# Optimization experiments

Measured on AMD Instinct MI355X. Metric: run time of the kernel, lower is better.

Reference implementation:

```python
import jax, jax.numpy as jnp
import numpy as np

WS = (4, 4, 4)          # window size (s, h, w)
NUM_HEADS = 6
DIM = 192               # kv channels C
CS = 2                  # channel_scale; q/out channels = DIM // CS
B = 256                 # num_windows * batch


def _rel_pos_index(ws):
    """Reproduces the module's relative_position_index buffer (shape [8shw, 2shw])."""
    s, h, w = ws
    cs = np.repeat(np.arange(s), 2)
    ch = np.repeat(np.arange(h), 2)
    cw = np.repeat(np.arange(w), 2)
    coords = np.stack(np.meshgrid(cs, ch, cw, indexing='ij'))   # (3, 2s, 2h, 2w)
    cf = coords.reshape(3, -1)                                   # (3, T), T = 8shw
    rel = cf[:, :, None] - cf[:, None, :]                        # (3, T, T)
    rel = rel[:, :, ::4]                                         # (3, T, T//4)
    rel = np.ascontiguousarray(rel.transpose(1, 2, 0))           # (T, T//4, 3)
    rel[:, :, 0] += s - 1
    rel[:, :, 1] += h - 1
    rel[:, :, 2] += w - 1
    rel[:, :, 0] *= 3 * h - 1
    rel[:, :, 1] *= 2 * h - 1
    return rel.sum(-1).astype(np.int32)                          # (T, T//4)


def setup_inputs() -> dict:
    key = jax.random.key(0)
    ks = jax.random.split(key, 9)
    s, h, w = WS
    qN = 8 * s * h * w          # 512 query tokens per window
    N = qN // 4                 # 128 key/value tokens per window
    C = DIM
    qC = DIM // CS
    table_len = (4 * s - 1) * (4 * h - 1) * (4 * w - 1)
    return {
        'kv': jax.random.normal(ks[0], (B, N, C), jnp.float32),
        'q': jax.random.normal(ks[1], (B, qN, qC), jnp.float32),
        'w_kv': jax.random.normal(ks[2], (C, 2 * C), jnp.float32) * 0.02,
        'b_kv': jnp.zeros((2 * C,), jnp.float32),
        'w_q': jax.random.normal(ks[3], (qC, C), jnp.float32) * 0.02,
        'b_q': jnp.zeros((C,), jnp.float32),
        'w_proj': jax.random.normal(ks[4], (C, qC), jnp.float32) * 0.02,
        'b_proj': jnp.zeros((qC,), jnp.float32),
        'bias_table': jax.random.normal(ks[5], (table_len, NUM_HEADS), jnp.float32) * 0.02,
        'rel_index': jnp.asarray(_rel_pos_index(WS)),
    }


def reference(kv, q, w_kv, b_kv, w_q, b_q, w_proj, b_proj, bias_table, rel_index):
    B_, N, C = kv.shape
    d = C // NUM_HEADS
    scale = d ** -0.5
    # project kv -> k, v : (B_, nH, N, d)
    kvp = (kv @ w_kv + b_kv).reshape(B_, N, 2, NUM_HEADS, d)
    k = kvp[:, :, 0].transpose(0, 2, 1, 3)
    v = kvp[:, :, 1].transpose(0, 2, 1, 3)
    # project q : (B_, nH, qN, d), pre-scaled
    qp = (q @ w_q + b_q).reshape(B_, -1, NUM_HEADS, d).transpose(0, 2, 1, 3) * scale
    attn = jnp.einsum('bhqd,bhkd->bhqk', qp, k)          # (B_, nH, qN, N)
    bias = bias_table[rel_index]                          # (qN, N, nH) gather
    attn = attn + bias.transpose(2, 0, 1)[None]           # + (1, nH, qN, N)
    attn = jax.nn.softmax(attn, axis=-1)
    out = jnp.einsum('bhqk,bhkd->bhqd', attn, v)          # (B_, nH, qN, d)
    out = out.transpose(0, 2, 1, 3).reshape(B_, -1, C)    # (B_, qN, C)
    return out @ w_proj + b_proj                          # (B_, qN, C//CS)
```

## Files before the change

### kernel.cpp

```cpp
#include <hip/hip_runtime.h>
#include <hip/hip_bf16.h>

#define B_    256
#define NKV   128
#define NQ    512
#define CDIM  192
#define QCDIM 96
#define NH    6
#define DH    32
#define SCALE 0.17677669529663687f

typedef __hip_bfloat16 bf16;
typedef __attribute__((ext_vector_type(8))) short s16x8;
typedef __attribute__((ext_vector_type(4))) float f32x4;
#define MFMA16(a, b, c) __builtin_amdgcn_mfma_f32_16x16x32_bf16(a, b, c, 0, 0, 0)

#define OFF_BIASF 0
#define OFF_WKVF  1572864
#define OFF_WQF   1720320
#define OFF_WPF   1757184
#define OFF_KF    1794048
#define OFF_VF    14376960

__global__ __launch_bounds__(256)
void precomp_all(const float* __restrict__ w_kv, const float* __restrict__ w_q,
                 const float* __restrict__ w_proj, const float* __restrict__ bias_table,
                 const int* __restrict__ rel_index,
                 float* __restrict__ biasF, bf16* __restrict__ wkvF,
                 bf16* __restrict__ wqF, bf16* __restrict__ wpF)
{
    const int i = blockIdx.x * 256 + threadIdx.x;
    if (i < 98304) {
        const int lane = i & 63, tl = (i >> 6) & 7, rowblk = (i >> 9) & 31, h = i >> 14;
        const int quad = lane >> 4, l16 = lane & 15;
        const int kvi = tl * 16 + l16;
        float vr[4];
        #pragma unroll
        for (int r = 0; r < 4; ++r) {
            const int qrow = rowblk * 16 + quad * 4 + r;
            vr[r] = bias_table[rel_index[qrow * NKV + kvi] * NH + h];
        }
        *(float4*)&biasF[i * 4] = make_float4(vr[0], vr[1], vr[2], vr[3]);
    } else if (i < 98304 + 73728) {
        const int i1 = i - 98304;
        const int j = i1 & 7, lane = (i1 >> 3) & 63, kk = (i1 >> 9) % 6, nt = i1 / 3072;
        const int quad = lane >> 4, l16 = lane & 15;
        wkvF[i1] = __float2bfloat16(w_kv[(kk * 32 + quad * 8 + j) * (2 * CDIM) + nt * 16 + l16]);
    } else if (i < 98304 + 92160) {
        const int i2 = i - 98304 - 73728;
        const int j = i2 & 7, lane = (i2 >> 3) & 63, kk = (i2 >> 9) % 3,
                  tl = (i2 / 1536) & 1, h = i2 / 3072;
        const int quad = lane >> 4, l16 = lane & 15;
        wqF[i2] = __float2bfloat16(w_q[(kk * 32 + quad * 8 + j) * CDIM + h * DH + tl * 16 + l16] * SCALE);
    } else {
        const int i3 = i - 98304 - 92160;
        const int j = i3 & 7, lane = (i3 >> 3) & 63, tn = (i3 >> 9) % 6, h = i3 / 3072;
        const int quad = lane >> 4, l16 = lane & 15;
        wpF[i3] = __float2bfloat16(w_proj[(h * DH + quad * 8 + j) * QCDIM + tn * 16 + l16]);
    }
}

__global__ __launch_bounds__(512, 4)
void proj_kv(const float* __restrict__ kv, const float* __restrict__ b_kv,
             const bf16* __restrict__ wkvF, bf16* __restrict__ KF, bf16* __restrict__ VF)
{
    __shared__ __align__(16) char smem[52224];
    bf16* sA = (bf16*)smem;
    const int b = blockIdx.x, half = blockIdx.y, t = threadIdx.x;
    const int w = t >> 6, lane = t & 63, quad = lane >> 4, l16 = lane & 15;
    const f32x4 ZV = {0.f, 0.f, 0.f, 0.f};

    for (int f = t; f < 6144; f += 512) {
        const int r = f / 48, c4 = f % 48;
        const float4 v = *(const float4*)&kv[((size_t)b * NKV + r) * CDIM + c4 * 4];
        __align__(8) bf16 tmp[4] = {__float2bfloat16(v.x), __float2bfloat16(v.y),
                                    __float2bfloat16(v.z), __float2bfloat16(v.w)};
        *(uint2*)&sA[r * 200 + c4 * 4] = *(uint2*)tmp;
    }
    __syncthreads();

    f32x4 acc[12];
    #pragma unroll
    for (int i = 0; i < 12; ++i) acc[i] = ZV;
    for (int kk = 0; kk < 6; ++kk) {
        const s16x8 a = *(const s16x8*)&sA[(w * 16 + l16) * 200 + kk * 32 + quad * 8];
        #pragma unroll
        for (int nt = 0; nt < 12; ++nt) {
            const s16x8 bb = *(const s16x8*)&wkvF[(((half * 12 + nt) * 6 + kk) * 64 + lane) * 8];
            acc[nt] = MFMA16(a, bb, acc[nt]);
        }
    }
    __syncthreads();

    if (half == 0) {
        bf16* bufK = (bf16*)smem;
        #pragma unroll
        for (int nt = 0; nt < 12; ++nt) {
            const int col = nt * 16 + l16;
            const float bias = b_kv[col];
            #pragma unroll
            for (int r = 0; r < 4; ++r)
                bufK[(w * 16 + quad * 4 + r) * 200 + col] = __float2bfloat16(acc[nt][r] + bias);
        }
        __syncthreads();
        bf16* KF_b = KF + (size_t)b * 24576;
        #pragma unroll
        for (int i = 0; i < 6; ++i) {
            const int fr = w * 6 + i, h = fr >> 3, tl = fr & 7;
            const s16x8 v = *(const s16x8*)&bufK[(tl * 16 + l16) * 200 + h * DH + quad * 8];
            *(s16x8*)&KF_b[(size_t)(fr * 64 + lane) * 8] = v;
        }
    } else {
        bf16* bufV = (bf16*)smem;
        #pragma unroll
        for (int nt = 0; nt < 12; ++nt) {
            const int d = nt * 16 + l16;
            const float bias = b_kv[CDIM + d];
            __align__(8) bf16 tmp[4];
            #pragma unroll
            for (int r = 0; r < 4; ++r) tmp[r] = __float2bfloat16(acc[nt][r] + bias);
            *(uint2*)&bufV[d * 136 + w * 16 + quad * 4] = *(uint2*)tmp;
        }
        __syncthreads();
        bf16* VF_b = VF + (size_t)b * 24576;
        #pragma unroll
        for (int i = 0; i < 6; ++i) {
            const int fr = w * 6 + i, h = fr >> 3, tl = (fr >> 2) & 1, kk = fr & 3;
            const s16x8 v = *(const s16x8*)&bufV[(h * DH + tl * 16 + l16) * 136 + kk * 32 + quad * 8];
            *(s16x8*)&VF_b[(size_t)(fr * 64 + lane) * 8] = v;
        }
    }
}

__global__ __launch_bounds__(256, 6)
void attn_fused(const float* __restrict__ q, const float* __restrict__ b_q,
                const float* __restrict__ b_proj, const char* __restrict__ wsro,
                float* __restrict__ out)
{
    __shared__ __align__(16) bf16 sP[4 * 16 * 136];
    const int b = blockIdx.x, y = blockIdx.y;
    const int t = threadIdx.x;
    const int w = t >> 6, lane = t & 63, quad = lane >> 4, l16 = lane & 15;

    const float* biasF = (const float*)(wsro + OFF_BIASF);
    const bf16*  wqF   = (const bf16*)(wsro + OFF_WQF);
    const bf16*  wpF   = (const bf16*)(wsro + OFF_WPF);
    const bf16*  KF_b  = (const bf16*)(wsro + OFF_KF) + (size_t)b * 24576;
    const bf16*  VF_b  = (const bf16*)(wsro + OFF_VF) + (size_t)b * 24576;

    const int rb = y * 4 + w;
    bf16* myP = sP + w * 2176;

    s16x8 qa[3];
    #pragma unroll
    for (int kk = 0; kk < 3; ++kk) {
        const float* src = &q[((size_t)b * NQ + rb * 16 + l16) * QCDIM + kk * 32 + quad * 8];
        const float4 a0 = *(const float4*)src;
        const float4 a1 = *(const float4*)(src + 4);
        __align__(16) bf16 tmp[8] = {
            __float2bfloat16(a0.x), __float2bfloat16(a0.y), __float2bfloat16(a0.z),
            __float2bfloat16(a0.w), __float2bfloat16(a1.x), __float2bfloat16(a1.y),
            __float2bfloat16(a1.z), __float2bfloat16(a1.w)};
        qa[kk] = *(s16x8*)tmp;
    }

    f32x4 outacc[6];
    #pragma unroll
    for (int tn = 0; tn < 6; ++tn) {
        const float bp = b_proj[tn * 16 + l16];
        outacc[tn] = (f32x4){bp, bp, bp, bp};
    }

    for (int h = 0; h < NH; ++h) {
        f32x4 qacc[2];
        #pragma unroll
        for (int tl = 0; tl < 2; ++tl) {
            const float bq = b_q[h * DH + tl * 16 + l16] * SCALE;
            qacc[tl] = (f32x4){bq, bq, bq, bq};
        }
        #pragma unroll
        for (int kk = 0; kk < 3; ++kk)
            #pragma unroll
            for (int tl = 0; tl < 2; ++tl) {
                const s16x8 bb = *(const s16x8*)&wqF[(((h * 2 + tl) * 3 + kk) * 64 + lane) * 8];
                qacc[tl] = MFMA16(qa[kk], bb, qacc[tl]);
            }
        #pragma unroll
        for (int tl = 0; tl < 2; ++tl)
            #pragma unroll
            for (int r = 0; r < 4; ++r)
                myP[(quad * 4 + r) * 136 + tl * 16 + l16] = __float2bfloat16(qacc[tl][r]);
        const s16x8 aQ = *(const s16x8*)&myP[l16 * 136 + quad * 8];

        float rs[4] = {0.f, 0.f, 0.f, 0.f};
        #pragma unroll
        for (int half = 0; half < 2; ++half) {
            f32x4 sacc[4];
            #pragma unroll
            for (int t4 = 0; t4 < 4; ++t4)
                sacc[t4] = *(const f32x4*)&biasF[(((h * 32 + rb) * 8 + half * 4 + t4) * 64 + lane) * 4];
            #pragma unroll
            for (int t4 = 0; t4 < 4; ++t4) {
                const s16x8 bb = *(const s16x8*)&KF_b[(size_t)((h * 8 + half * 4 + t4) * 64 + lane) * 8];
                sacc[t4] = MFMA16(aQ, bb, sacc[t4]);
            }
            #pragma unroll
            for (int t4 = 0; t4 < 4; ++t4)
                #pragma unroll
                for (int r = 0; r < 4; ++r) {
                    const float vv = __expf(sacc[t4][r]);
                    rs[r] += vv;
                    myP[(quad * 4 + r) * 136 + (half * 4 + t4) * 16 + l16] = __float2bfloat16(vv);
                }
        }
        float inv[4];
        #pragma unroll
        for (int r = 0; r < 4; ++r) {
            float s = rs[r];
            #pragma unroll
            for (int off = 1; off < 16; off <<= 1) s += __shfl_xor(s, off, 16);
            inv[r] = 1.f / s;
        }

        f32x4 oacc[2];
        oacc[0] = (f32x4){0.f, 0.f, 0.f, 0.f};
        oacc[1] = (f32x4){0.f, 0.f, 0.f, 0.f};
        #pragma unroll
        for (int kk = 0; kk < 4; ++kk) {
            const s16x8 aP = *(const s16x8*)&myP[l16 * 136 + kk * 32 + quad * 8];
            #pragma unroll
            for (int tl = 0; tl < 2; ++tl) {
                const s16x8 bb = *(const s16x8*)&VF_b[(size_t)(((h * 2 + tl) * 4 + kk) * 64 + lane) * 8];
                oacc[tl] = MFMA16(aP, bb, oacc[tl]);
            }
        }
        #pragma unroll
        for (int tl = 0; tl < 2; ++tl)
            #pragma unroll
            for (int r = 0; r < 4; ++r)
                myP[(quad * 4 + r) * 136 + tl * 16 + l16] = __float2bfloat16(oacc[tl][r] * inv[r]);

        const s16x8 aO = *(const s16x8*)&myP[l16 * 136 + quad * 8];
        #pragma unroll
        for (int tn = 0; tn < 6; ++tn) {
            const s16x8 bb = *(const s16x8*)&wpF[((h * 6 + tn) * 64 + lane) * 8];
            outacc[tn] = MFMA16(aO, bb, outacc[tn]);
        }
    }

    #pragma unroll
    for (int tn = 0; tn < 6; ++tn)
        #pragma unroll
        for (int r = 0; r < 4; ++r)
            out[((size_t)b * NQ + rb * 16 + quad * 4 + r) * QCDIM + tn * 16 + l16]
                = outacc[tn][r];
}

extern "C" void kernel_launch(void* const* d_in, const int* in_sizes, int n_in,
                              void* d_out, int out_size, void* d_ws, size_t ws_size,
                              hipStream_t stream)
{
    const float* kv       = (const float*)d_in[0];
    const float* q        = (const float*)d_in[1];
    const float* w_kv     = (const float*)d_in[2];
    const float* b_kv     = (const float*)d_in[3];
    const float* w_q      = (const float*)d_in[4];
    const float* b_q      = (const float*)d_in[5];
    const float* w_proj   = (const float*)d_in[6];
    const float* b_proj   = (const float*)d_in[7];
    const float* bias_tab = (const float*)d_in[8];
    const int*   rel_idx  = (const int*)d_in[9];
    char* ws = (char*)d_ws;

    precomp_all<<<816, 256, 0, stream>>>(w_kv, w_q, w_proj, bias_tab, rel_idx,
                                         (float*)(ws + OFF_BIASF), (bf16*)(ws + OFF_WKVF),
                                         (bf16*)(ws + OFF_WQF), (bf16*)(ws + OFF_WPF));
    proj_kv<<<dim3(B_, 2), 512, 0, stream>>>(kv, b_kv, (const bf16*)(ws + OFF_WKVF),
                                             (bf16*)(ws + OFF_KF), (bf16*)(ws + OFF_VF));
    attn_fused<<<dim3(B_, 8), 256, 0, stream>>>(q, b_q, b_proj, (const char*)ws,
                                                (float*)d_out);
}
```

Before: 249.7 us.

## Split attention heads across waves and use exp2 with log2e-folded scale

Each attention block now handles one 16-row query block, with one wave per head (384 threads), in place of one wave looping over all six heads. Per-head outputs go into shared memory, and after a barrier each wave computes one 16-column slice of the output projection. The intent is to raise parallelism and shorten the serial per-wave head loop, at the cost of a block-wide sync and 6x redundant q loads per row block. Separately, log2(e) is folded into the precomputed bias and the q weights so the softmax can use the native exp2 instruction.

```diff
diff --git a/kernel.cpp b/kernel.cpp
--- a/kernel.cpp
+++ b/kernel.cpp
@@ -9,6 +9,7 @@
 #define NH    6
 #define DH    32
 #define SCALE 0.17677669529663687f
+#define LOG2E 1.4426950408889634f
 
 typedef __hip_bfloat16 bf16;
 typedef __attribute__((ext_vector_type(8))) short s16x8;
@@ -38,7 +39,7 @@
         #pragma unroll
         for (int r = 0; r < 4; ++r) {
             const int qrow = rowblk * 16 + quad * 4 + r;
-            vr[r] = bias_table[rel_index[qrow * NKV + kvi] * NH + h];
+            vr[r] = bias_table[rel_index[qrow * NKV + kvi] * NH + h] * LOG2E;
         }
         *(float4*)&biasF[i * 4] = make_float4(vr[0], vr[1], vr[2], vr[3]);
     } else if (i < 98304 + 73728) {
@@ -51,7 +52,8 @@
         const int j = i2 & 7, lane = (i2 >> 3) & 63, kk = (i2 >> 9) % 3,
                   tl = (i2 / 1536) & 1, h = i2 / 3072;
         const int quad = lane >> 4, l16 = lane & 15;
-        wqF[i2] = __float2bfloat16(w_q[(kk * 32 + quad * 8 + j) * CDIM + h * DH + tl * 16 + l16] * SCALE);
+        wqF[i2] = __float2bfloat16(w_q[(kk * 32 + quad * 8 + j) * CDIM + h * DH + tl * 16 + l16]
+                                   * (SCALE * LOG2E));
     } else {
         const int i3 = i - 98304 - 92160;
         const int j = i3 & 7, lane = (i3 >> 3) & 63, tn = (i3 >> 9) % 6, h = i3 / 3072;
@@ -132,15 +134,16 @@
     }
 }
 
-__global__ __launch_bounds__(256, 6)
+__global__ __launch_bounds__(384, 6)
 void attn_fused(const float* __restrict__ q, const float* __restrict__ b_q,
                 const float* __restrict__ b_proj, const char* __restrict__ wsro,
                 float* __restrict__ out)
 {
-    __shared__ __align__(16) bf16 sP[4 * 16 * 136];
-    const int b = blockIdx.x, y = blockIdx.y;
+    __shared__ __align__(16) bf16 sP[6 * 16 * 136];
+    __shared__ __align__(16) bf16 sO[16 * 200];
+    const int b = blockIdx.x, rb = blockIdx.y;
     const int t = threadIdx.x;
-    const int w = t >> 6, lane = t & 63, quad = lane >> 4, l16 = lane & 15;
+    const int h = t >> 6, lane = t & 63, quad = lane >> 4, l16 = lane & 15;
 
     const float* biasF = (const float*)(wsro + OFF_BIASF);
     const bf16*  wqF   = (const bf16*)(wsro + OFF_WQF);
@@ -148,10 +151,14 @@
     const bf16*  KF_b  = (const bf16*)(wsro + OFF_KF) + (size_t)b * 24576;
     const bf16*  VF_b  = (const bf16*)(wsro + OFF_VF) + (size_t)b * 24576;
 
-    const int rb = y * 4 + w;
-    bf16* myP = sP + w * 2176;
-
-    s16x8 qa[3];
+    bf16* myP = sP + h * 2176;
+
+    f32x4 qacc[2];
+    #pragma unroll
+    for (int tl = 0; tl < 2; ++tl) {
+        const float bq = b_q[h * DH + tl * 16 + l16] * (SCALE * LOG2E);
+        qacc[tl] = (f32x4){bq, bq, bq, bq};
+    }
     #pragma unroll
     for (int kk = 0; kk < 3; ++kk) {
         const float* src = &q[((size_t)b * NQ + rb * 16 + l16) * QCDIM + kk * 32 + quad * 8];
@@ -161,99 +168,84 @@
             __float2bfloat16(a0.x), __float2bfloat16(a0.y), __float2bfloat16(a0.z),
             __float2bfloat16(a0.w), __float2bfloat16(a1.x), __float2bfloat16(a1.y),
             __float2bfloat16(a1.z), __float2bfloat16(a1.w)};
-        qa[kk] = *(s16x8*)tmp;
-    }
-
-    f32x4 outacc[6];
-    #pragma unroll
-    for (int tn = 0; tn < 6; ++tn) {
-        const float bp = b_proj[tn * 16 + l16];
-        outacc[tn] = (f32x4){bp, bp, bp, bp};
-    }
-
-    for (int h = 0; h < NH; ++h) {
-        f32x4 qacc[2];
+        const s16x8 qa = *(s16x8*)tmp;
         #pragma unroll
         for (int tl = 0; tl < 2; ++tl) {
-            const float bq = b_q[h * DH + tl * 16 + l16] * SCALE;
-            qacc[tl] = (f32x4){bq, bq, bq, bq};
-        }
-        #pragma unroll
-        for (int kk = 0; kk < 3; ++kk)
+            const s16x8 bb = *(const s16x8*)&wqF[(((h * 2 + tl) * 3 + kk) * 64 + lane) * 8];
+            qacc[tl] = MFMA16(qa, bb, qacc[tl]);
+        }
+    }
+    #pragma unroll
+    for (int tl = 0; tl < 2; ++tl)
+        #pragma unroll
+        for (int r = 0; r < 4; ++r)
+            myP[(quad * 4 + r) * 136 + tl * 16 + l16] = __float2bfloat16(qacc[tl][r]);
+    const s16x8 aQ = *(const s16x8*)&myP[l16 * 136 + quad * 8];
+
+    float rs[4] = {0.f, 0.f, 0.f, 0.f};
+    #pragma unroll
+    for (int half = 0; half < 2; ++half) {
+        f32x4 sacc[4];
+        #pragma unroll
+        for (int t4 = 0; t4 < 4; ++t4)
+            sacc[t4] = *(const f32x4*)&biasF[(((h * 32 + rb) * 8 + half * 4 + t4) * 64 + lane) * 4];
+        #pragma unroll
+        for (int t4 = 0; t4 < 4; ++t4) {
+            const s16x8 bb = *(const s16x8*)&KF_b[(size_t)((h * 8 + half * 4 + t4) * 64 + lane) * 8];
+            sacc[t4] = MFMA16(aQ, bb, sacc[t4]);
+        }
+        #pragma unroll
+        for (int t4 = 0; t4 < 4; ++t4)
             #pragma unroll
-            for (int tl = 0; tl < 2; ++tl) {
-                const s16x8 bb = *(const s16x8*)&wqF[(((h * 2 + tl) * 3 + kk) * 64 + lane) * 8];
-                qacc[tl] = MFMA16(qa[kk], bb, qacc[tl]);
+            for (int r = 0; r < 4; ++r) {
+                const float vv = __builtin_amdgcn_exp2f(sacc[t4][r]);
+                rs[r] += vv;
+                myP[(quad * 4 + r) * 136 + (half * 4 + t4) * 16 + l16] = __float2bfloat16(vv);
             }
-        #pragma unroll
-        for (int tl = 0; tl < 2; ++tl)
-            #pragma unroll
-            for (int r = 0; r < 4; ++r)
-                myP[(quad * 4 + r) * 136 + tl * 16 + l16] = __float2bfloat16(qacc[tl][r]);
-        const s16x8 aQ = *(const s16x8*)&myP[l16 * 136 + quad * 8];
-
-        float rs[4] = {0.f, 0.f, 0.f, 0.f};
-        #pragma unroll
-        for (int half = 0; half < 2; ++half) {
-            f32x4 sacc[4];
-            #pragma unroll
-            for (int t4 = 0; t4 < 4; ++t4)
-                sacc[t4] = *(const f32x4*)&biasF[(((h * 32 + rb) * 8 + half * 4 + t4) * 64 + lane) * 4];
-            #pragma unroll
-            for (int t4 = 0; t4 < 4; ++t4) {
-                const s16x8 bb = *(const s16x8*)&KF_b[(size_t)((h * 8 + half * 4 + t4) * 64 + lane) * 8];
-                sacc[t4] = MFMA16(aQ, bb, sacc[t4]);
-            }
-            #pragma unroll
-            for (int t4 = 0; t4 < 4; ++t4)
-                #pragma unroll
-                for (int r = 0; r < 4; ++r) {
-                    const float vv = __expf(sacc[t4][r]);
-                    rs[r] += vv;
-                    myP[(quad * 4 + r) * 136 + (half * 4 + t4) * 16 + l16] = __float2bfloat16(vv);
-                }
-        }
-        float inv[4];
-        #pragma unroll
-        for (int r = 0; r < 4; ++r) {
-            float s = rs[r];
-            #pragma unroll
-            for (int off = 1; off < 16; off <<= 1) s += __shfl_xor(s, off, 16);
-            inv[r] = 1.f / s;
-        }
-
-        f32x4 oacc[2];
-        oacc[0] = (f32x4){0.f, 0.f, 0.f, 0.f};
-        oacc[1] = (f32x4){0.f, 0.f, 0.f, 0.f};
-        #pragma unroll
-        for (int kk = 0; kk < 4; ++kk) {
-            const s16x8 aP = *(const s16x8*)&myP[l16 * 136 + kk * 32 + quad * 8];
-            #pragma unroll
-            for (int tl = 0; tl < 2; ++tl) {
-                const s16x8 bb = *(const s16x8*)&VF_b[(size_t)(((h * 2 + tl) * 4 + kk) * 64 + lane) * 8];
-                oacc[tl] = MFMA16(aP, bb, oacc[tl]);
-            }
-        }
-        #pragma unroll
-        for (int tl = 0; tl < 2; ++tl)
-            #pragma unroll
-            for (int r = 0; r < 4; ++r)
-                myP[(quad * 4 + r) * 136 + tl * 16 + l16] = __float2bfloat16(oacc[tl][r] * inv[r]);
-
-        const s16x8 aO = *(const s16x8*)&myP[l16 * 136 + quad * 8];
-        #pragma unroll
-        for (int tn = 0; tn < 6; ++tn) {
-            const s16x8 bb = *(const s16x8*)&wpF[((h * 6 + tn) * 64 + lane) * 8];
-            outacc[tn] = MFMA16(aO, bb, outacc[tn]);
-        }
-    }
-
-    #pragma unroll
-    for (int tn = 0; tn < 6; ++tn)
+    }
+    float inv[4];
+    #pragma unroll
+    for (int r = 0; r < 4; ++r) {
+        float s = rs[r];
+        #pragma unroll
+        for (int off = 1; off < 16; off <<= 1) s += __shfl_xor(s, off, 16);
+        inv[r] = 1.f / s;
+    }
+
+    f32x4 oacc[2];
+    oacc[0] = (f32x4){0.f, 0.f, 0.f, 0.f};
+    oacc[1] = (f32x4){0.f, 0.f, 0.f, 0.f};
+    #pragma unroll
+    for (int kk = 0; kk < 4; ++kk) {
+        const s16x8 aP = *(const s16x8*)&myP[l16 * 136 + kk * 32 + quad * 8];
+        #pragma unroll
+        for (int tl = 0; tl < 2; ++tl) {
+            const s16x8 bb = *(const s16x8*)&VF_b[(size_t)(((h * 2 + tl) * 4 + kk) * 64 + lane) * 8];
+            oacc[tl] = MFMA16(aP, bb, oacc[tl]);
+        }
+    }
+    #pragma unroll
+    for (int tl = 0; tl < 2; ++tl)
         #pragma unroll
         for (int r = 0; r < 4; ++r)
-            out[((size_t)b * NQ + rb * 16 + quad * 4 + r) * QCDIM + tn * 16 + l16]
-                = outacc[tn][r];
+            sO[(quad * 4 + r) * 200 + h * DH + tl * 16 + l16] = __float2bfloat16(oacc[tl][r] * inv[r]);
+
+    __syncthreads();
+
+    f32x4 acc;
+    {
+        const float bp = b_proj[h * 16 + l16];
+        acc = (f32x4){bp, bp, bp, bp};
+    }
+    #pragma unroll
+    for (int kk = 0; kk < 6; ++kk) {
+        const s16x8 aO = *(const s16x8*)&sO[l16 * 200 + kk * 32 + quad * 8];
+        const s16x8 bb = *(const s16x8*)&wpF[((kk * 6 + h) * 64 + lane) * 8];
+        acc = MFMA16(aO, bb, acc);
+    }
+    #pragma unroll
+    for (int r = 0; r < 4; ++r)
+        out[((size_t)b * NQ + rb * 16 + quad * 4 + r) * QCDIM + h * 16 + l16] = acc[r];
 }
 
 extern "C" void kernel_launch(void* const* d_in, const int* in_sizes, int n_in,
@@ -277,6 +269,6 @@
                                          (bf16*)(ws + OFF_WQF), (bf16*)(ws + OFF_WPF));
     proj_kv<<<dim3(B_, 2), 512, 0, stream>>>(kv, b_kv, (const bf16*)(ws + OFF_WKVF),
                                              (bf16*)(ws + OFF_KF), (bf16*)(ws + OFF_VF));
-    attn_fused<<<dim3(B_, 8), 256, 0, stream>>>(q, b_q, b_proj, (const char*)ws,
-                                                (float*)d_out);
-}
+    attn_fused<<<dim3(B_, 32), 384, 0, stream>>>(q, b_q, b_proj, (const char*)ws,
+                                                 (float*)d_out);
+}
```

Result: faster. 242.4 us (-2.9%).

## Prefetch per-head operands into registers, store bias as bf16, use exp2

Applied to the files above, without the earlier changes.

Stores the gathered relative-position bias as bf16 instead of fp32, which halves its footprint, and folds log2(e) into the bias and the Q weights so softmax can use the native exp2 instruction. In the attention kernel, all K, V, Wq, Wproj and bias fragments for a head are loaded into registers up front rather than interleaved with the MFMAs, so memory latency can overlap compute. To fit the extra registers, the occupancy hint drops from 6 to 4 blocks per CU. The risks are less latency hiding from lower occupancy and bf16 rounding of the bias.

```diff
diff --git a/kernel.cpp b/kernel.cpp
--- a/kernel.cpp
+++ b/kernel.cpp
@@ -9,24 +9,30 @@
 #define NH    6
 #define DH    32
 #define SCALE 0.17677669529663687f
+#define LOG2E 1.4426950408889634f
 
 typedef __hip_bfloat16 bf16;
 typedef __attribute__((ext_vector_type(8))) short s16x8;
+typedef __attribute__((ext_vector_type(4))) short s16x4;
 typedef __attribute__((ext_vector_type(4))) float f32x4;
 #define MFMA16(a, b, c) __builtin_amdgcn_mfma_f32_16x16x32_bf16(a, b, c, 0, 0, 0)
 
+__device__ __forceinline__ float b2f(short s) {
+    return __uint_as_float(((unsigned)(unsigned short)s) << 16);
+}
+
 #define OFF_BIASF 0
-#define OFF_WKVF  1572864
-#define OFF_WQF   1720320
-#define OFF_WPF   1757184
-#define OFF_KF    1794048
-#define OFF_VF    14376960
+#define OFF_WKVF  786432
+#define OFF_WQF   933888
+#define OFF_WPF   970752
+#define OFF_KF    1007616
+#define OFF_VF    13590528
 
 __global__ __launch_bounds__(256)
 void precomp_all(const float* __restrict__ w_kv, const float* __restrict__ w_q,
                  const float* __restrict__ w_proj, const float* __restrict__ bias_table,
                  const int* __restrict__ rel_index,
-                 float* __restrict__ biasF, bf16* __restrict__ wkvF,
+                 bf16* __restrict__ biasF, bf16* __restrict__ wkvF,
                  bf16* __restrict__ wqF, bf16* __restrict__ wpF)
 {
     const int i = blockIdx.x * 256 + threadIdx.x;
@@ -34,13 +40,13 @@
         const int lane = i & 63, tl = (i >> 6) & 7, rowblk = (i >> 9) & 31, h = i >> 14;
         const int quad = lane >> 4, l16 = lane & 15;
         const int kvi = tl * 16 + l16;
-        float vr[4];
+        __align__(8) bf16 vr[4];
         #pragma unroll
         for (int r = 0; r < 4; ++r) {
             const int qrow = rowblk * 16 + quad * 4 + r;
-            vr[r] = bias_table[rel_index[qrow * NKV + kvi] * NH + h];
-        }
-        *(float4*)&biasF[i * 4] = make_float4(vr[0], vr[1], vr[2], vr[3]);
+            vr[r] = __float2bfloat16(bias_table[rel_index[qrow * NKV + kvi] * NH + h] * LOG2E);
+        }
+        *(uint2*)&biasF[i * 4] = *(uint2*)vr;
     } else if (i < 98304 + 73728) {
         const int i1 = i - 98304;
         const int j = i1 & 7, lane = (i1 >> 3) & 63, kk = (i1 >> 9) % 6, nt = i1 / 3072;
@@ -51,7 +57,8 @@
         const int j = i2 & 7, lane = (i2 >> 3) & 63, kk = (i2 >> 9) % 3,
                   tl = (i2 / 1536) & 1, h = i2 / 3072;
         const int quad = lane >> 4, l16 = lane & 15;
-        wqF[i2] = __float2bfloat16(w_q[(kk * 32 + quad * 8 + j) * CDIM + h * DH + tl * 16 + l16] * SCALE);
+        wqF[i2] = __float2bfloat16(w_q[(kk * 32 + quad * 8 + j) * CDIM + h * DH + tl * 16 + l16]
+                                   * (SCALE * LOG2E));
     } else {
         const int i3 = i - 98304 - 92160;
         const int j = i3 & 7, lane = (i3 >> 3) & 63, tn = (i3 >> 9) % 6, h = i3 / 3072;
@@ -132,7 +139,7 @@
     }
 }
 
-__global__ __launch_bounds__(256, 6)
+__global__ __launch_bounds__(256, 4)
 void attn_fused(const float* __restrict__ q, const float* __restrict__ b_q,
                 const float* __restrict__ b_proj, const char* __restrict__ wsro,
                 float* __restrict__ out)
@@ -142,11 +149,11 @@
     const int t = threadIdx.x;
     const int w = t >> 6, lane = t & 63, quad = lane >> 4, l16 = lane & 15;
 
-    const float* biasF = (const float*)(wsro + OFF_BIASF);
-    const bf16*  wqF   = (const bf16*)(wsro + OFF_WQF);
-    const bf16*  wpF   = (const bf16*)(wsro + OFF_WPF);
-    const bf16*  KF_b  = (const bf16*)(wsro + OFF_KF) + (size_t)b * 24576;
-    const bf16*  VF_b  = (const bf16*)(wsro + OFF_VF) + (size_t)b * 24576;
+    const bf16* biasF = (const bf16*)(wsro + OFF_BIASF);
+    const bf16* wqF   = (const bf16*)(wsro + OFF_WQF);
+    const bf16* wpF   = (const bf16*)(wsro + OFF_WPF);
+    const bf16* KF_b  = (const bf16*)(wsro + OFF_KF) + (size_t)b * 24576;
+    const bf16* VF_b  = (const bf16*)(wsro + OFF_VF) + (size_t)b * 24576;
 
     const int rb = y * 4 + w;
     bf16* myP = sP + w * 2176;
@@ -172,47 +179,67 @@
     }
 
     for (int h = 0; h < NH; ++h) {
+        s16x8 kf[8];
+        #pragma unroll
+        for (int t4 = 0; t4 < 8; ++t4)
+            kf[t4] = *(const s16x8*)&KF_b[(size_t)((h * 8 + t4) * 64 + lane) * 8];
+        s16x4 bb[8];
+        #pragma unroll
+        for (int t4 = 0; t4 < 8; ++t4)
+            bb[t4] = *(const s16x4*)&biasF[(((h * 32 + rb) * 8 + t4) * 64 + lane) * 4];
+        s16x8 wqf[6];
+        #pragma unroll
+        for (int i = 0; i < 6; ++i)
+            wqf[i] = *(const s16x8*)&wqF[((h * 6 + i) * 64 + lane) * 8];
+
         f32x4 qacc[2];
         #pragma unroll
         for (int tl = 0; tl < 2; ++tl) {
-            const float bq = b_q[h * DH + tl * 16 + l16] * SCALE;
+            const float bq = b_q[h * DH + tl * 16 + l16] * (SCALE * LOG2E);
             qacc[tl] = (f32x4){bq, bq, bq, bq};
         }
         #pragma unroll
         for (int kk = 0; kk < 3; ++kk)
             #pragma unroll
-            for (int tl = 0; tl < 2; ++tl) {
-                const s16x8 bb = *(const s16x8*)&wqF[(((h * 2 + tl) * 3 + kk) * 64 + lane) * 8];
-                qacc[tl] = MFMA16(qa[kk], bb, qacc[tl]);
-            }
+            for (int tl = 0; tl < 2; ++tl)
+                qacc[tl] = MFMA16(qa[kk], wqf[tl * 3 + kk], qacc[tl]);
         #pragma unroll
         for (int tl = 0; tl < 2; ++tl)
             #pragma unroll
             for (int r = 0; r < 4; ++r)
                 myP[(quad * 4 + r) * 136 + tl * 16 + l16] = __float2bfloat16(qacc[tl][r]);
+
+        s16x8 vf[8];
+        #pragma unroll
+        for (int i = 0; i < 8; ++i)
+            vf[i] = *(const s16x8*)&VF_b[(size_t)((h * 8 + i) * 64 + lane) * 8];
+
         const s16x8 aQ = *(const s16x8*)&myP[l16 * 136 + quad * 8];
 
+        f32x4 sacc[8];
+        #pragma unroll
+        for (int t4 = 0; t4 < 8; ++t4)
+            #pragma unroll
+            for (int r = 0; r < 4; ++r)
+                sacc[t4][r] = b2f(bb[t4][r]);
+        #pragma unroll
+        for (int t4 = 0; t4 < 8; ++t4)
+            sacc[t4] = MFMA16(aQ, kf[t4], sacc[t4]);
         float rs[4] = {0.f, 0.f, 0.f, 0.f};
         #pragma unroll
-        for (int half = 0; half < 2; ++half) {
-            f32x4 sacc[4];
-            #pragma unroll
-            for (int t4 = 0; t4 < 4; ++t4)
-                sacc[t4] = *(const f32x4*)&biasF[(((h * 32 + rb) * 8 + half * 4 + t4) * 64 + lane) * 4];
-            #pragma unroll
-            for (int t4 = 0; t4 < 4; ++t4) {
-                const s16x8 bb = *(const s16x8*)&KF_b[(size_t)((h * 8 + half * 4 + t4) * 64 + lane) * 8];
-                sacc[t4] = MFMA16(aQ, bb, sacc[t4]);
+        for (int t4 = 0; t4 < 8; ++t4)
+            #pragma unroll
+            for (int r = 0; r < 4; ++r) {
+                const float vv = __builtin_amdgcn_exp2f(sacc[t4][r]);
+                rs[r] += vv;
+                myP[(quad * 4 + r) * 136 + t4 * 16 + l16] = __float2bfloat16(vv);
             }
-            #pragma unroll
-            for (int t4 = 0; t4 < 4; ++t4)
-                #pragma unroll
-                for (int r = 0; r < 4; ++r) {
-                    const float vv = __expf(sacc[t4][r]);
-                    rs[r] += vv;
-                    myP[(quad * 4 + r) * 136 + (half * 4 + t4) * 16 + l16] = __float2bfloat16(vv);
-                }
-        }
+
+        s16x8 wpf[6];
+        #pragma unroll
+        for (int i = 0; i < 6; ++i)
+            wpf[i] = *(const s16x8*)&wpF[((h * 6 + i) * 64 + lane) * 8];
+
         float inv[4];
         #pragma unroll
         for (int r = 0; r < 4; ++r) {
@@ -229,10 +256,8 @@
         for (int kk = 0; kk < 4; ++kk) {
             const s16x8 aP = *(const s16x8*)&myP[l16 * 136 + kk * 32 + quad * 8];
             #pragma unroll
-            for (int tl = 0; tl < 2; ++tl) {
-                const s16x8 bb = *(const s16x8*)&VF_b[(size_t)(((h * 2 + tl) * 4 + kk) * 64 + lane) * 8];
-                oacc[tl] = MFMA16(aP, bb, oacc[tl]);
-            }
+            for (int tl = 0; tl < 2; ++tl)
+                oacc[tl] = MFMA16(aP, vf[tl * 4 + kk], oacc[tl]);
         }
         #pragma unroll
         for (int tl = 0; tl < 2; ++tl)
@@ -242,10 +267,8 @@
 
         const s16x8 aO = *(const s16x8*)&myP[l16 * 136 + quad * 8];
         #pragma unroll
-        for (int tn = 0; tn < 6; ++tn) {
-            const s16x8 bb = *(const s16x8*)&wpF[((h * 6 + tn) * 64 + lane) * 8];
-            outacc[tn] = MFMA16(aO, bb, outacc[tn]);
-        }
+        for (int tn = 0; tn < 6; ++tn)
+            outacc[tn] = MFMA16(aO, wpf[tn], outacc[tn]);
     }
 
     #pragma unroll
@@ -273,7 +296,7 @@
     char* ws = (char*)d_ws;
 
     precomp_all<<<816, 256, 0, stream>>>(w_kv, w_q, w_proj, bias_tab, rel_idx,
-                                         (float*)(ws + OFF_BIASF), (bf16*)(ws + OFF_WKVF),
+                                         (bf16*)(ws + OFF_BIASF), (bf16*)(ws + OFF_WKVF),
                                          (bf16*)(ws + OFF_WQF), (bf16*)(ws + OFF_WPF));
     proj_kv<<<dim3(B_, 2), 512, 0, stream>>>(kv, b_kv, (const bf16*)(ws + OFF_WKVF),
                                              (bf16*)(ws + OFF_KF), (bf16*)(ws + OFF_VF));
```

Result: faster. 210.8 us (-15.6%).
